# Performance work log

Hardware: AMD Instinct MI355X
Metric: run time of the kernel (lower is better)

Reference implementation:

```python
import jax, jax.numpy as jnp
import numpy as np

DIM = 256
HEADS = 8
DIM_HEAD = 64
INNER = HEADS * DIM_HEAD  # 512
SCALE = DIM_HEAD ** -0.5
EPS = 1e-5


def _layernorm(x, w, b):
    mu = jnp.mean(x, axis=-1, keepdims=True)
    var = jnp.var(x, axis=-1, keepdims=True)
    return (x - mu) * jax.lax.rsqrt(var + EPS) * w + b


def setup_inputs() -> dict:
    key = jax.random.key(0)
    ks = jax.random.split(key, 20)
    B, N, M, H, W = 8, 4096, 256, 64, 64
    s = 0.02
    inp = {
        "feat": jax.random.normal(ks[0], (B, N, DIM), jnp.float32),
        "center": jax.random.normal(ks[1], (B, M, DIM), jnp.float32),
        "pos": jax.random.normal(ks[2], (B, DIM, H, W), jnp.float32),
        "center_pos": jax.random.normal(ks[3], (B, M, DIM), jnp.float32),
        # projection weights stored [in, out] so y = x @ W
        "Wq": jax.random.normal(ks[4], (DIM, INNER), jnp.float32) * s,
        "Wk": jax.random.normal(ks[5], (DIM, INNER), jnp.float32) * s,
        "Wv1": jax.random.normal(ks[6], (DIM, INNER), jnp.float32) * s,
        "Wv2": jax.random.normal(ks[7], (DIM, INNER), jnp.float32) * s,
        "Wo1": jax.random.normal(ks[8], (INNER, DIM), jnp.float32) * s,
        "Wo2": jax.random.normal(ks[9], (INNER, DIM), jnp.float32) * s,
        "ln1_w": jnp.ones((DIM,), jnp.float32),
        "ln1_b": jnp.zeros((DIM,), jnp.float32),
        "ln2_w": jnp.ones((DIM,), jnp.float32),
        "ln2_b": jnp.zeros((DIM,), jnp.float32),
        "ffn1_W1": jax.random.normal(ks[10], (DIM, DIM), jnp.float32) * s,
        "ffn1_W2": jax.random.normal(ks[11], (DIM, DIM), jnp.float32) * s,
        "ffn1_b2": jnp.zeros((DIM,), jnp.float32),
        "ffn2_W1": jax.random.normal(ks[12], (DIM, DIM), jnp.float32) * s,
        "ffn2_W2": jax.random.normal(ks[13], (DIM, DIM), jnp.float32) * s,
        "ffn2_b2": jnp.zeros((DIM,), jnp.float32),
    }
    return inp


def reference(feat, center, pos, center_pos, Wq, Wk, Wv1, Wv2, Wo1, Wo2,
              ln1_w, ln1_b, ln2_w, ln2_b, ffn1_W1, ffn1_W2, ffn1_b2,
              ffn2_W1, ffn2_W2, ffn2_b2):
    B = feat.shape[0]
    # pos: [B, C, H, W] -> [B, N, C]
    pos_f = pos.reshape(B, DIM, -1).transpose(0, 2, 1)
    q = (feat + pos_f) @ Wq            # [B, N, INNER]
    k = (center + center_pos) @ Wk     # [B, M, INNER]
    v1 = feat @ Wv1                    # [B, N, INNER]
    v2 = center @ Wv2                  # [B, M, INNER]

    def split(x):  # [B, T, h*d] -> [B, h, T, d]
        return x.reshape(B, x.shape[1], HEADS, DIM_HEAD).transpose(0, 2, 1, 3)

    q, k, v1, v2 = split(q), split(k), split(v1), split(v2)
    attn = jnp.einsum("bhnd,bhmd->bhnm", q, k) * SCALE  # [B, h, N, M]
    attn1 = jax.nn.softmax(attn, axis=-2)  # over N (queries)
    attn2 = jax.nn.softmax(attn, axis=-1)  # over M (keys)
    out_feat = jnp.einsum("bhnm,bhmd->bhnd", attn2, v2)    # [B, h, N, d]
    out_center = jnp.einsum("bhnm,bhnd->bhmd", attn1, v1)  # [B, h, M, d]

    def merge(x):  # [B, h, T, d] -> [B, T, h*d]
        return x.transpose(0, 2, 1, 3).reshape(B, x.shape[2], INNER)

    out_feat = merge(out_feat) @ Wo1 + feat
    out_center = merge(out_center) @ Wo2 + center
    out_feat = _layernorm(out_feat, ln1_w, ln1_b)
    out_center = _layernorm(out_center, ln2_w, ln2_b)
    out_feat = jax.nn.relu(out_feat @ ffn1_W1) @ ffn1_W2 + ffn1_b2 + out_feat
    out_center = jax.nn.relu(out_center @ ffn2_W1) @ ffn2_W2 + ffn2_b2 + out_center
    return out_feat, out_center
```

## Files before the change

### kernel.cpp

```cpp
#include <hip/hip_runtime.h>

typedef __bf16 bf16;
typedef __bf16 bf16x4 __attribute__((ext_vector_type(4)));
typedef __bf16 bf16x8 __attribute__((ext_vector_type(8)));
typedef float f32x4 __attribute__((ext_vector_type(4)));

#define MFMA16(a, b, c) __builtin_amdgcn_mfma_f32_16x16x32_bf16(a, b, c, 0, 0, 0)

#define CEXP 0.18033688011112042f

struct WTArgs {
  const float* src[10];
  bf16* dst[10];
  int K[10];
  int N[10];
};

__global__ __launch_bounds__(256) void wtrans_kernel(WTArgs args) {
  const int z = blockIdx.z;
  const int K = args.K[z], N = args.N[z];
  const int k0 = blockIdx.x * 64, n0 = blockIdx.y * 64;
  if (k0 >= K || n0 >= N) return;
  __shared__ float t[64][65];
  const int tx = threadIdx.x & 63, ty = threadIdx.x >> 6;
  const float* __restrict__ src = args.src[z];
  bf16* __restrict__ dst = args.dst[z];
#pragma unroll
  for (int i = 0; i < 16; ++i)
    t[ty + i * 4][tx] = src[(size_t)(k0 + ty + i * 4) * N + n0 + tx];
  __syncthreads();
#pragma unroll
  for (int i = 0; i < 16; ++i)
    dst[(size_t)(n0 + ty + i * 4) * K + k0 + tx] = (bf16)t[tx][ty + i * 4];
}

__global__ __launch_bounds__(256) void prep_xq_kernel(
    const float* __restrict__ feat, const float* __restrict__ pos,
    bf16* __restrict__ xq) {
  const int n0 = blockIdx.x * 64;
  const int c0 = blockIdx.y * 64;
  const int b = blockIdx.z;
  __shared__ float t[64][65];
  const int tx = threadIdx.x & 63, ty = threadIdx.x >> 6;
#pragma unroll
  for (int i = 0; i < 16; ++i) {
    int c = ty + i * 4;
    t[c][tx] = pos[((size_t)b * 256 + c0 + c) * 4096 + n0 + tx];
  }
  __syncthreads();
#pragma unroll
  for (int i = 0; i < 16; ++i) {
    int n = ty + i * 4;
    size_t off = ((size_t)b * 4096 + n0 + n) * 256 + c0 + tx;
    xq[off] = (bf16)(feat[off] + t[tx][n]);
  }
}

__device__ inline void stage16(const bf16* g, bf16* l) {
  __builtin_amdgcn_global_load_lds(
      (const __attribute__((address_space(1))) void*)g,
      (__attribute__((address_space(3))) void*)l, 16, 0, 0);
}
__device__ inline void stage16(const float* g, bf16* l) {
  f32x4 u = *(const f32x4*)g;
  f32x4 v = *((const f32x4*)g + 1);
  bf16x8 o;
#pragma unroll
  for (int i = 0; i < 4; ++i) {
    o[i] = (bf16)u[i];
    o[4 + i] = (bf16)v[i];
  }
  *(bf16x8*)l = o;
}
__device__ inline void stage16(const float* g, const float* g2, bf16* l) {
  f32x4 u = *(const f32x4*)g + *(const f32x4*)g2;
  f32x4 v = *((const f32x4*)g + 1) + *((const f32x4*)g2 + 1);
  bf16x8 o;
#pragma unroll
  for (int i = 0; i < 4; ++i) {
    o[i] = (bf16)u[i];
    o[4 + i] = (bf16)v[i];
  }
  *(bf16x8*)l = o;
}

__device__ inline f32x4 rload(const float* p) { return *(const f32x4*)p; }
__device__ inline f32x4 rload(const bf16* p) {
  bf16x4 t = *(const bf16x4*)p;
  return (f32x4){(float)t[0], (float)t[1], (float)t[2], (float)t[3]};
}
__device__ inline void cstore(float* p, f32x4 v) { *(f32x4*)p = v; }
__device__ inline void cstore(bf16* p, f32x4 v) {
  bf16x4 o;
  o[0] = (bf16)v[0]; o[1] = (bf16)v[1]; o[2] = (bf16)v[2]; o[3] = (bf16)v[3];
  *(bf16x4*)p = o;
}

struct GArg {
  const void* A[2];
  const void* A2[2];
  const bf16* BT[2];
  void* C[2];
  const void* resid[2];
  const float* bias[2];
  int M[2];
};

template <int EPI, typename TO, typename TR, typename TA, bool FUSE2>
__global__ __launch_bounds__(256) void gemm_kernel(GArg g, int N, int K) {
  const int z = blockIdx.z;
  const int m0 = blockIdx.x * 128;
  if (m0 >= g.M[z]) return;
  const TA* A = (const TA*)g.A[z];
  const TA* A2 = (const TA*)g.A2[z];
  const bf16* BT = g.BT[z];
  TO* C = (TO*)g.C[z];
  const TR* resid = (const TR*)g.resid[z];
  const float* bias = g.bias[z];

  const int n0 = blockIdx.y * 128;
  const int tid = threadIdx.x;
  const int lane = tid & 63;
  const int w = tid >> 6;
  const int wr = (w >> 1) * 64, wc = (w & 1) * 64;
  const int l15 = lane & 15, quad = lane >> 4;

  __shared__ __align__(16) bf16 Al[128 * 32];
  __shared__ __align__(16) bf16 Bl[128 * 32];

  f32x4 acc[4][4];
#pragma unroll
  for (int i = 0; i < 4; ++i)
#pragma unroll
    for (int j = 0; j < 4; ++j) acc[i][j] = (f32x4){0.f, 0.f, 0.f, 0.f};

  const int sw = (((l15 >> 1) & 3) ^ quad) * 8;

  for (int k0 = 0; k0 < K; k0 += 32) {
#pragma unroll
    for (int c = 0; c < 2; ++c) {
      int idx = tid + c * 256;
      int row = idx >> 2;
      int gs = ((idx & 3) ^ ((row >> 1) & 3)) * 8;
      size_t aoff = (size_t)(m0 + row) * K + k0 + gs;
      if constexpr (FUSE2)
        stage16(A + aoff, A2 + aoff, Al + idx * 8);
      else
        stage16(A + aoff, Al + idx * 8);
      stage16(BT + (size_t)(n0 + row) * K + k0 + gs, Bl + idx * 8);
    }
    __syncthreads();
    bf16x8 fa[4], fb[4];
#pragma unroll
    for (int i = 0; i < 4; ++i) {
      fa[i] = *(const bf16x8*)(Al + (wr + i * 16 + l15) * 32 + sw);
      fb[i] = *(const bf16x8*)(Bl + (wc + i * 16 + l15) * 32 + sw);
    }
#pragma unroll
    for (int i = 0; i < 4; ++i)
#pragma unroll
      for (int j = 0; j < 4; ++j)
        acc[i][j] = MFMA16(fb[j], fa[i], acc[i][j]);
    __syncthreads();
  }

#pragma unroll
  for (int i = 0; i < 4; ++i) {
#pragma unroll
    for (int j = 0; j < 4; ++j) {
      int row = m0 + wr + i * 16 + l15;
      int col = n0 + wc + j * 16 + quad * 4;
      size_t off = (size_t)row * N + col;
      f32x4 v = acc[i][j];
      if constexpr (EPI == 1) {
#pragma unroll
        for (int e = 0; e < 4; ++e) v[e] = fmaxf(v[e], 0.f);
      }
      if constexpr (EPI == 2) v += rload(resid + off);
      if constexpr (EPI == 3)
        v += rload(resid + off) + *(const f32x4*)(bias + col);
      cstore(C + off, v);
    }
  }
}

__global__ __launch_bounds__(256, 1) void attf_kernel(
    const bf16* q, const bf16* __restrict__ kk, const bf16* __restrict__ v1,
    const bf16* __restrict__ v2, bf16* af, float* __restrict__ acc_p,
    float* __restrict__ colsum_p) {
  const int nb = blockIdx.x;
  const int h = blockIdx.y;
  const int b = blockIdx.z;
  const int tid = threadIdx.x;
  const int lane = tid & 63;
  const int w = tid >> 6;
  const int l15 = lane & 15, quad = lane >> 4;

  __shared__ __align__(16) bf16 klds[256 * 72];
  __shared__ __align__(16) bf16 v2T[64 * 264];
  __shared__ __align__(16) bf16 v1T[2][64 * 72];
  __shared__ __align__(16) bf16 PT[256 * 72];
  __shared__ __align__(16) bf16 Pl[4][16 * 264];

#pragma unroll
  for (int c = 0; c < 8; ++c) {
    int idx = tid + c * 256;
    int m = idx >> 3;
    int dc = (idx & 7) * 8;
    *(bf16x8*)(klds + m * 72 + dc) =
        *(const bf16x8*)(kk + ((size_t)(b * 256 + m)) * 512 + h * 64 + dc);
  }
#pragma unroll
  for (int c = 0; c < 8; ++c) {
    int idx = tid + c * 256;
    int m = idx >> 3;
    int dc = (idx & 7) * 8;
    bf16x8 t =
        *(const bf16x8*)(v2 + ((size_t)(b * 256 + m)) * 512 + h * 64 + dc);
#pragma unroll
    for (int j = 0; j < 8; ++j) v2T[(dc + j) * 264 + m] = t[j];
  }
  {
    const int nl = tid >> 3;
    const int dc = (tid & 7) * 8;
    const bf16* v1b =
        v1 + ((size_t)(b * 4096 + nb * 1024)) * 512 + h * 64 + dc;
    bf16x8 t0 = *(const bf16x8*)(v1b + (size_t)nl * 512);
    bf16x8 t1 = *(const bf16x8*)(v1b + (size_t)(nl + 32) * 512);
#pragma unroll
    for (int j = 0; j < 8; ++j) {
      v1T[0][(dc + j) * 72 + nl] = t0[j];
      v1T[0][(dc + j) * 72 + nl + 32] = t1[j];
    }
  }
  bf16x8 qa0, qa1;
  {
    int nrow = b * 4096 + nb * 1024 + w * 16 + l15;
    const bf16* qp = q + (size_t)nrow * 512 + h * 64 + quad * 8;
    qa0 = *(const bf16x8*)(qp);
    qa1 = *(const bf16x8*)(qp + 32);
  }

  f32x4 oc2[16];
#pragma unroll
  for (int i = 0; i < 16; ++i) oc2[i] = (f32x4){0.f, 0.f, 0.f, 0.f};
  float cs[16];
#pragma unroll
  for (int i = 0; i < 16; ++i) cs[i] = 0.f;

  __syncthreads();

#pragma unroll 2
  for (int ch = 0; ch < 16; ++ch) {
    bf16x8 v1a, v1b;
    const int nl = tid >> 3;
    const int dc = (tid & 7) * 8;
    if (ch < 15) {
      const bf16* v1p =
          v1 + ((size_t)(b * 4096 + nb * 1024 + (ch + 1) * 64)) * 512 +
          h * 64 + dc;
      v1a = *(const bf16x8*)(v1p + (size_t)nl * 512);
      v1b = *(const bf16x8*)(v1p + (size_t)(nl + 32) * 512);
    }

    float rs[4] = {0.f, 0.f, 0.f, 0.f};
#pragma unroll
    for (int mt = 0; mt < 16; ++mt) {
      const bf16* kp = klds + (mt * 16 + l15) * 72 + quad * 8;
      bf16x8 b0 = *(const bf16x8*)(kp);
      bf16x8 b1 = *(const bf16x8*)(kp + 32);
      f32x4 s = (f32x4){0.f, 0.f, 0.f, 0.f};
      s = MFMA16(qa0, b0, s);
      s = MFMA16(qa1, b1, s);
      float e0 = exp2f(s[0] * CEXP);
      float e1 = exp2f(s[1] * CEXP);
      float e2 = exp2f(s[2] * CEXP);
      float e3 = exp2f(s[3] * CEXP);
      rs[0] += e0; rs[1] += e1; rs[2] += e2; rs[3] += e3;
      cs[mt] += e0 + e1 + e2 + e3;
      Pl[w][(quad * 4 + 0) * 264 + mt * 16 + l15] = (bf16)e0;
      Pl[w][(quad * 4 + 1) * 264 + mt * 16 + l15] = (bf16)e1;
      Pl[w][(quad * 4 + 2) * 264 + mt * 16 + l15] = (bf16)e2;
      Pl[w][(quad * 4 + 3) * 264 + mt * 16 + l15] = (bf16)e3;
      bf16x4 ev;
      ev[0] = (bf16)e0; ev[1] = (bf16)e1; ev[2] = (bf16)e2; ev[3] = (bf16)e3;
      *(bf16x4*)(PT + (mt * 16 + l15) * 72 + w * 16 + quad * 4) = ev;
    }
    if (ch < 15) {
      bf16* dst = v1T[(ch + 1) & 1];
#pragma unroll
      for (int j = 0; j < 8; ++j) {
        dst[(dc + j) * 72 + nl] = v1a[j];
        dst[(dc + j) * 72 + nl + 32] = v1b[j];
      }
    }
    __syncthreads();

    bf16x8 qn0 = qa0, qn1 = qa1;
    if (ch < 15) {
      int nrow = b * 4096 + nb * 1024 + (ch + 1) * 64 + w * 16 + l15;
      const bf16* qp = q + (size_t)nrow * 512 + h * 64 + quad * 8;
      qn0 = *(const bf16x8*)(qp);
      qn1 = *(const bf16x8*)(qp + 32);
    }

    f32x4 o1[4];
#pragma unroll
    for (int i = 0; i < 4; ++i) o1[i] = (f32x4){0.f, 0.f, 0.f, 0.f};
#pragma unroll
    for (int ks = 0; ks < 8; ++ks) {
      bf16x8 pa = *(const bf16x8*)(Pl[w] + l15 * 264 + ks * 32 + quad * 8);
#pragma unroll
      for (int dt = 0; dt < 4; ++dt) {
        bf16x8 vb = *(const bf16x8*)(v2T + (dt * 16 + l15) * 264 + ks * 32 +
                                     quad * 8);
        o1[dt] = MFMA16(vb, pa, o1[dt]);
      }
    }
#pragma unroll
    for (int r = 0; r < 4; ++r) {
      float v = rs[r];
      v += __shfl_xor(v, 1, 64);
      v += __shfl_xor(v, 2, 64);
      v += __shfl_xor(v, 4, 64);
      v += __shfl_xor(v, 8, 64);
      rs[r] = v;
    }
    {
      int srcq = (l15 >> 2) << 4;
      float s0 = __shfl(rs[0], srcq, 64);
      float s1 = __shfl(rs[1], srcq, 64);
      float s2 = __shfl(rs[2], srcq, 64);
      float s3 = __shfl(rs[3], srcq, 64);
      float a01 = (l15 & 1) ? s1 : s0;
      float a23 = (l15 & 1) ? s3 : s2;
      float inv = 1.f / ((l15 & 2) ? a23 : a01);
      int n = nb * 1024 + ch * 64 + w * 16 + l15;
      bf16* ap = af + ((size_t)(b * 4096 + n)) * 512 + h * 64 + quad * 4;
#pragma unroll
      for (int dt = 0; dt < 4; ++dt) {
        bf16x4 ov;
        ov[0] = (bf16)(o1[dt][0] * inv);
        ov[1] = (bf16)(o1[dt][1] * inv);
        ov[2] = (bf16)(o1[dt][2] * inv);
        ov[3] = (bf16)(o1[dt][3] * inv);
        *(bf16x4*)(ap + dt * 16) = ov;
      }
    }

    const bf16* vc = v1T[ch & 1];
#pragma unroll
    for (int ks = 0; ks < 2; ++ks) {
      bf16x8 vbv[4];
#pragma unroll
      for (int dt = 0; dt < 4; ++dt)
        vbv[dt] = *(const bf16x8*)(vc + (dt * 16 + l15) * 72 + ks * 32 +
                                   quad * 8);
#pragma unroll
      for (int mq = 0; mq < 4; ++mq) {
        bf16x8 pa2 = *(const bf16x8*)(PT + (mq * 64 + w * 16 + l15) * 72 +
                                      ks * 32 + quad * 8);
#pragma unroll
        for (int dt = 0; dt < 4; ++dt)
          oc2[mq * 4 + dt] = MFMA16(vbv[dt], pa2, oc2[mq * 4 + dt]);
      }
    }
    __syncthreads();
    qa0 = qn0;
    qa1 = qn1;
  }

  float* cw = (float*)klds;
#pragma unroll
  for (int t = 0; t < 16; ++t) {
    float v = cs[t];
    v += __shfl_xor(v, 16, 64);
    v += __shfl_xor(v, 32, 64);
    if (quad == 0) cw[w * 256 + t * 16 + l15] = v;
  }
  __syncthreads();
  {
    int m = tid;
    float s = cw[m] + cw[256 + m] + cw[512 + m] + cw[768 + m];
    colsum_p[((size_t)(nb * 64 + b * 8 + h)) * 256 + m] = s;
  }
  float* base = acc_p + ((size_t)(nb * 64 + b * 8 + h)) * 256 * 64;
#pragma unroll
  for (int mq = 0; mq < 4; ++mq) {
    int m = mq * 64 + w * 16 + l15;
#pragma unroll
    for (int dt = 0; dt < 4; ++dt)
      *(f32x4*)(base + m * 64 + dt * 16 + quad * 4) = oc2[mq * 4 + dt];
  }
}

__global__ __launch_bounds__(256) void acm_kernel(
    const float* __restrict__ acc_p, const float* __restrict__ colsum_p,
    bf16* __restrict__ acm) {
  int idx = blockIdx.x * 256 + threadIdx.x;
  int d = idx & 63;
  int h = (idx >> 6) & 7;
  int m = (idx >> 9) & 255;
  int b = idx >> 17;
  float cv = 0.f, v = 0.f;
#pragma unroll
  for (int p = 0; p < 4; ++p) {
    cv += colsum_p[((size_t)(p * 64 + b * 8 + h)) * 256 + m];
    v += acc_p[(((size_t)(p * 64 + b * 8 + h)) * 256 + m) * 64 + d];
  }
  acm[idx] = (bf16)(v / cv);
}

__global__ __launch_bounds__(256) void ln_kernel(
    const bf16* __restrict__ x0, const bf16* __restrict__ x1,
    const float* __restrict__ w0, const float* __restrict__ b0,
    const float* __restrict__ w1, const float* __restrict__ b1,
    bf16* __restrict__ y0, bf16* __restrict__ y1, int rows0, int rows1) {
  int wave = threadIdx.x >> 6;
  int lane = threadIdx.x & 63;
  int row = blockIdx.x * 4 + wave;
  const bf16* x;
  const float *wv, *bv;
  bf16* y;
  if (row < rows0) {
    x = x0; wv = w0; bv = b0; y = y0;
  } else {
    row -= rows0;
    if (row >= rows1) return;
    x = x1; wv = w1; bv = b1; y = y1;
  }
  const bf16* xr = x + (size_t)row * 256;
  bf16x4 v = *(const bf16x4*)(xr + lane * 4);
  float f0 = v[0], f1 = v[1], f2 = v[2], f3 = v[3];
  float s = f0 + f1 + f2 + f3;
  float ss = f0 * f0 + f1 * f1 + f2 * f2 + f3 * f3;
#pragma unroll
  for (int m = 1; m < 64; m <<= 1) {
    s += __shfl_xor(s, m, 64);
    ss += __shfl_xor(ss, m, 64);
  }
  float mean = s * (1.f / 256.f);
  float var = ss * (1.f / 256.f) - mean * mean;
  float rstd = rsqrtf(var + 1e-5f);
  f32x4 wq = *(const f32x4*)(wv + lane * 4);
  f32x4 bq = *(const f32x4*)(bv + lane * 4);
  bf16x4 o;
  o[0] = (bf16)((f0 - mean) * rstd * wq[0] + bq[0]);
  o[1] = (bf16)((f1 - mean) * rstd * wq[1] + bq[1]);
  o[2] = (bf16)((f2 - mean) * rstd * wq[2] + bq[2]);
  o[3] = (bf16)((f3 - mean) * rstd * wq[3] + bq[3]);
  *(bf16x4*)(y + (size_t)row * 256 + lane * 4) = o;
}

extern "C" void kernel_launch(void* const* d_in, const int* in_sizes, int n_in,
                              void* d_out, int out_size, void* d_ws,
                              size_t ws_size, hipStream_t stream) {
  const float* feat = (const float*)d_in[0];
  const float* center = (const float*)d_in[1];
  const float* pos = (const float*)d_in[2];
  const float* cpos = (const float*)d_in[3];
  const float* Wq = (const float*)d_in[4];
  const float* Wk = (const float*)d_in[5];
  const float* Wv1 = (const float*)d_in[6];
  const float* Wv2 = (const float*)d_in[7];
  const float* Wo1 = (const float*)d_in[8];
  const float* Wo2 = (const float*)d_in[9];
  const float* ln1w = (const float*)d_in[10];
  const float* ln1b = (const float*)d_in[11];
  const float* ln2w = (const float*)d_in[12];
  const float* ln2b = (const float*)d_in[13];
  const float* f1W1 = (const float*)d_in[14];
  const float* f1W2 = (const float*)d_in[15];
  const float* f1b2 = (const float*)d_in[16];
  const float* f2W1 = (const float*)d_in[17];
  const float* f2W2 = (const float*)d_in[18];
  const float* f2b2 = (const float*)d_in[19];

  char* ws = (char*)d_ws;
  const size_t MB = 1024 * 1024;
  bf16* q_ = (bf16*)(ws + 0);
  bf16* af_ = q_;
  bf16* v1_ = (bf16*)(ws + 32 * MB);
  bf16* xq_ = (bf16*)(ws + 64 * MB);
  float* accp_ = (float*)(ws + 64 * MB);
  bf16* rf_ = xq_;
  bf16* k_ = (bf16*)(ws + 80 * MB);
  bf16* rc_ = (bf16*)(ws + 82 * MB);
  bf16* v2_ = (bf16*)(ws + 83 * MB);
  bf16* acm_ = v2_;
  float* colsum_ = (float*)(ws + 89 * MB);
  bf16* wt_ = (bf16*)(ws + 89 * MB + 262144);
  bf16* yf_ = q_;
  bf16* tf_ = (bf16*)(ws + 16 * MB);
  bf16* yc_ = (bf16*)(ws + 92 * MB);
  bf16* tc_ = (bf16*)(ws + 93 * MB);

  bf16* WqT = wt_;
  bf16* WkT = WqT + 131072;
  bf16* Wv1T = WkT + 131072;
  bf16* Wv2T = Wv1T + 131072;
  bf16* Wo1T = Wv2T + 131072;
  bf16* Wo2T = Wo1T + 131072;
  bf16* f1W1T = Wo2T + 131072;
  bf16* f1W2T = f1W1T + 65536;
  bf16* f2W1T = f1W2T + 65536;
  bf16* f2W2T = f2W1T + 65536;

  float* out_feat = (float*)d_out;
  float* out_center = out_feat + (size_t)8 * 4096 * 256;

  WTArgs wa;
  const float* srcs[10] = {Wq, Wk, Wv1, Wv2, Wo1, Wo2, f1W1, f1W2, f2W1, f2W2};
  bf16* dsts[10] = {WqT, WkT, Wv1T, Wv2T, Wo1T, Wo2T, f1W1T, f1W2T, f2W1T, f2W2T};
  int Ks[10] = {256, 256, 256, 256, 512, 512, 256, 256, 256, 256};
  int Ns[10] = {512, 512, 512, 512, 256, 256, 256, 256, 256, 256};
  for (int i = 0; i < 10; ++i) {
    wa.src[i] = srcs[i];
    wa.dst[i] = dsts[i];
    wa.K[i] = Ks[i];
    wa.N[i] = Ns[i];
  }

  wtrans_kernel<<<dim3(8, 8, 10), 256, 0, stream>>>(wa);
  prep_xq_kernel<<<dim3(64, 4, 8), 256, 0, stream>>>(feat, pos, xq_);

  {
    GArg a{};
    a.A[0] = xq_; a.BT[0] = WqT; a.C[0] = q_; a.M[0] = 32768;
    gemm_kernel<0, bf16, bf16, bf16, false>
        <<<dim3(256, 4, 1), 256, 0, stream>>>(a, 512, 256);
  }
  {
    GArg a{};
    a.A[0] = center; a.A2[0] = cpos; a.BT[0] = WkT; a.C[0] = k_;
    a.M[0] = 2048;
    gemm_kernel<0, bf16, bf16, float, true>
        <<<dim3(16, 4, 1), 256, 0, stream>>>(a, 512, 256);
  }
  {
    GArg a{};
    a.A[0] = feat; a.A[1] = center;
    a.BT[0] = Wv1T; a.BT[1] = Wv2T;
    a.C[0] = v1_; a.C[1] = v2_;
    a.M[0] = 32768; a.M[1] = 2048;
    gemm_kernel<0, bf16, bf16, float, false>
        <<<dim3(256, 4, 2), 256, 0, stream>>>(a, 512, 256);
  }

  attf_kernel<<<dim3(4, 8, 8), 256, 0, stream>>>(q_, k_, v1_, v2_, af_, accp_,
                                                 colsum_);
  acm_kernel<<<dim3(4096), 256, 0, stream>>>(accp_, colsum_, acm_);

  {
    GArg a{};
    a.A[0] = af_; a.A[1] = acm_;
    a.BT[0] = Wo1T; a.BT[1] = Wo2T;
    a.C[0] = rf_; a.C[1] = rc_;
    a.resid[0] = feat; a.resid[1] = center;
    a.M[0] = 32768; a.M[1] = 2048;
    gemm_kernel<2, bf16, float, bf16, false>
        <<<dim3(256, 2, 2), 256, 0, stream>>>(a, 256, 512);
  }
  ln_kernel<<<dim3(8704), 256, 0, stream>>>(rf_, rc_, ln1w, ln1b, ln2w, ln2b,
                                            yf_, yc_, 32768, 2048);
  {
    GArg a{};
    a.A[0] = yf_; a.A[1] = yc_;
    a.BT[0] = f1W1T; a.BT[1] = f2W1T;
    a.C[0] = tf_; a.C[1] = tc_;
    a.M[0] = 32768; a.M[1] = 2048;
    gemm_kernel<1, bf16, bf16, bf16, false>
        <<<dim3(256, 2, 2), 256, 0, stream>>>(a, 256, 256);
  }
  {
    GArg a{};
    a.A[0] = tf_; a.A[1] = tc_;
    a.BT[0] = f1W2T; a.BT[1] = f2W2T;
    a.C[0] = out_feat; a.C[1] = out_center;
    a.resid[0] = yf_; a.resid[1] = yc_;
    a.bias[0] = f1b2; a.bias[1] = f2b2;
    a.M[0] = 32768; a.M[1] = 2048;
    gemm_kernel<3, float, bf16, bf16, false>
        <<<dim3(256, 2, 2), 256, 0, stream>>>(a, 256, 256);
  }
}
```

Before: 379.6 us.

## Double-buffer GEMM LDS tiles and keep attention probabilities in registers

The GEMM kernel now double-buffers its A/B LDS tiles, so each k-step needs one barrier instead of two and the next tile's loads can overlap the MFMAs. In the attention kernel the S MFMA operands are swapped so each lane holds the probabilities it needs for the P·V2 product in registers. v2T is stored with a permuted column order to match, and the Pl shared buffer and the cross-lane row-sum shuffles are removed. Column sums are now computed by an MFMA against a ones vector instead of per-lane accumulation plus an LDS reduction, at the cost of extra MFMAs and higher register pressure.

```diff
diff --git a/kernel.cpp b/kernel.cpp
--- a/kernel.cpp
+++ b/kernel.cpp
@@ -125,8 +125,8 @@
   const int wr = (w >> 1) * 64, wc = (w & 1) * 64;
   const int l15 = lane & 15, quad = lane >> 4;
 
-  __shared__ __align__(16) bf16 Al[128 * 32];
-  __shared__ __align__(16) bf16 Bl[128 * 32];
+  __shared__ __align__(16) bf16 Al[2][128 * 32];
+  __shared__ __align__(16) bf16 Bl[2][128 * 32];
 
   f32x4 acc[4][4];
 #pragma unroll
@@ -136,7 +136,7 @@
 
   const int sw = (((l15 >> 1) & 3) ^ quad) * 8;
 
-  for (int k0 = 0; k0 < K; k0 += 32) {
+  auto stage = [&](int buf, int k0) {
 #pragma unroll
     for (int c = 0; c < 2; ++c) {
       int idx = tid + c * 256;
@@ -144,24 +144,31 @@
       int gs = ((idx & 3) ^ ((row >> 1) & 3)) * 8;
       size_t aoff = (size_t)(m0 + row) * K + k0 + gs;
       if constexpr (FUSE2)
-        stage16(A + aoff, A2 + aoff, Al + idx * 8);
+        stage16(A + aoff, A2 + aoff, Al[buf] + idx * 8);
       else
-        stage16(A + aoff, Al + idx * 8);
-      stage16(BT + (size_t)(n0 + row) * K + k0 + gs, Bl + idx * 8);
-    }
+        stage16(A + aoff, Al[buf] + idx * 8);
+      stage16(BT + (size_t)(n0 + row) * K + k0 + gs, Bl[buf] + idx * 8);
+    }
+  };
+
+  stage(0, 0);
+  int cur = 0;
+  const int nt = K >> 5;
+  for (int t = 0; t < nt; ++t) {
     __syncthreads();
+    if (t + 1 < nt) stage(cur ^ 1, (t + 1) * 32);
     bf16x8 fa[4], fb[4];
 #pragma unroll
     for (int i = 0; i < 4; ++i) {
-      fa[i] = *(const bf16x8*)(Al + (wr + i * 16 + l15) * 32 + sw);
-      fb[i] = *(const bf16x8*)(Bl + (wc + i * 16 + l15) * 32 + sw);
+      fa[i] = *(const bf16x8*)(Al[cur] + (wr + i * 16 + l15) * 32 + sw);
+      fb[i] = *(const bf16x8*)(Bl[cur] + (wc + i * 16 + l15) * 32 + sw);
     }
 #pragma unroll
     for (int i = 0; i < 4; ++i)
 #pragma unroll
       for (int j = 0; j < 4; ++j)
         acc[i][j] = MFMA16(fb[j], fa[i], acc[i][j]);
-    __syncthreads();
+    cur ^= 1;
   }
 
 #pragma unroll
@@ -200,7 +207,6 @@
   __shared__ __align__(16) bf16 v2T[64 * 264];
   __shared__ __align__(16) bf16 v1T[2][64 * 72];
   __shared__ __align__(16) bf16 PT[256 * 72];
-  __shared__ __align__(16) bf16 Pl[4][16 * 264];
 
 #pragma unroll
   for (int c = 0; c < 8; ++c) {
@@ -217,8 +223,10 @@
     int dc = (idx & 7) * 8;
     bf16x8 t =
         *(const bf16x8*)(v2 + ((size_t)(b * 256 + m)) * 512 + h * 64 + dc);
-#pragma unroll
-    for (int j = 0; j < 8; ++j) v2T[(dc + j) * 264 + m] = t[j];
+    int p = (m & ~31) |
+            (((((m >> 2) & 3) << 3) + (m & 3)) + (((m >> 4) & 1) << 2));
+#pragma unroll
+    for (int j = 0; j < 8; ++j) v2T[(dc + j) * 264 + p] = t[j];
   }
   {
     const int nl = tid >> 3;
@@ -244,13 +252,15 @@
   f32x4 oc2[16];
 #pragma unroll
   for (int i = 0; i < 16; ++i) oc2[i] = (f32x4){0.f, 0.f, 0.f, 0.f};
-  float cs[16];
-#pragma unroll
-  for (int i = 0; i < 16; ++i) cs[i] = 0.f;
+  f32x4 csa[4];
+#pragma unroll
+  for (int i = 0; i < 4; ++i) csa[i] = (f32x4){0.f, 0.f, 0.f, 0.f};
+  bf16x8 ones8;
+#pragma unroll
+  for (int j = 0; j < 8; ++j) ones8[j] = (bf16)1.0f;
 
   __syncthreads();
 
-#pragma unroll 2
   for (int ch = 0; ch < 16; ++ch) {
     bf16x8 v1a, v1b;
     const int nl = tid >> 3;
@@ -263,45 +273,31 @@
       v1b = *(const bf16x8*)(v1p + (size_t)(nl + 32) * 512);
     }
 
-    float rs[4] = {0.f, 0.f, 0.f, 0.f};
+    bf16x8 pa[8];
+    float rs = 0.f;
 #pragma unroll
     for (int mt = 0; mt < 16; ++mt) {
       const bf16* kp = klds + (mt * 16 + l15) * 72 + quad * 8;
-      bf16x8 b0 = *(const bf16x8*)(kp);
-      bf16x8 b1 = *(const bf16x8*)(kp + 32);
+      bf16x8 ka0 = *(const bf16x8*)(kp);
+      bf16x8 ka1 = *(const bf16x8*)(kp + 32);
       f32x4 s = (f32x4){0.f, 0.f, 0.f, 0.f};
-      s = MFMA16(qa0, b0, s);
-      s = MFMA16(qa1, b1, s);
+      s = MFMA16(ka0, qa0, s);
+      s = MFMA16(ka1, qa1, s);
       float e0 = exp2f(s[0] * CEXP);
       float e1 = exp2f(s[1] * CEXP);
       float e2 = exp2f(s[2] * CEXP);
       float e3 = exp2f(s[3] * CEXP);
-      rs[0] += e0; rs[1] += e1; rs[2] += e2; rs[3] += e3;
-      cs[mt] += e0 + e1 + e2 + e3;
-      Pl[w][(quad * 4 + 0) * 264 + mt * 16 + l15] = (bf16)e0;
-      Pl[w][(quad * 4 + 1) * 264 + mt * 16 + l15] = (bf16)e1;
-      Pl[w][(quad * 4 + 2) * 264 + mt * 16 + l15] = (bf16)e2;
-      Pl[w][(quad * 4 + 3) * 264 + mt * 16 + l15] = (bf16)e3;
-      bf16x4 ev;
-      ev[0] = (bf16)e0; ev[1] = (bf16)e1; ev[2] = (bf16)e2; ev[3] = (bf16)e3;
-      *(bf16x4*)(PT + (mt * 16 + l15) * 72 + w * 16 + quad * 4) = ev;
-    }
-    if (ch < 15) {
-      bf16* dst = v1T[(ch + 1) & 1];
-#pragma unroll
-      for (int j = 0; j < 8; ++j) {
-        dst[(dc + j) * 72 + nl] = v1a[j];
-        dst[(dc + j) * 72 + nl + 32] = v1b[j];
-      }
-    }
-    __syncthreads();
-
-    bf16x8 qn0 = qa0, qn1 = qa1;
-    if (ch < 15) {
-      int nrow = b * 4096 + nb * 1024 + (ch + 1) * 64 + w * 16 + l15;
-      const bf16* qp = q + (size_t)nrow * 512 + h * 64 + quad * 8;
-      qn0 = *(const bf16x8*)(qp);
-      qn1 = *(const bf16x8*)(qp + 32);
+      rs += (e0 + e1) + (e2 + e3);
+      bf16 b0 = (bf16)e0, b1 = (bf16)e1, b2 = (bf16)e2, b3 = (bf16)e3;
+      int mrow = mt * 16 + quad * 4;
+      PT[(mrow + 0) * 72 + w * 16 + l15] = b0;
+      PT[(mrow + 1) * 72 + w * 16 + l15] = b1;
+      PT[(mrow + 2) * 72 + w * 16 + l15] = b2;
+      PT[(mrow + 3) * 72 + w * 16 + l15] = b3;
+      pa[mt >> 1][(mt & 1) * 4 + 0] = b0;
+      pa[mt >> 1][(mt & 1) * 4 + 1] = b1;
+      pa[mt >> 1][(mt & 1) * 4 + 2] = b2;
+      pa[mt >> 1][(mt & 1) * 4 + 3] = b3;
     }
 
     f32x4 o1[4];
@@ -309,32 +305,17 @@
     for (int i = 0; i < 4; ++i) o1[i] = (f32x4){0.f, 0.f, 0.f, 0.f};
 #pragma unroll
     for (int ks = 0; ks < 8; ++ks) {
-      bf16x8 pa = *(const bf16x8*)(Pl[w] + l15 * 264 + ks * 32 + quad * 8);
 #pragma unroll
       for (int dt = 0; dt < 4; ++dt) {
         bf16x8 vb = *(const bf16x8*)(v2T + (dt * 16 + l15) * 264 + ks * 32 +
                                      quad * 8);
-        o1[dt] = MFMA16(vb, pa, o1[dt]);
+        o1[dt] = MFMA16(vb, pa[ks], o1[dt]);
       }
     }
-#pragma unroll
-    for (int r = 0; r < 4; ++r) {
-      float v = rs[r];
-      v += __shfl_xor(v, 1, 64);
-      v += __shfl_xor(v, 2, 64);
-      v += __shfl_xor(v, 4, 64);
-      v += __shfl_xor(v, 8, 64);
-      rs[r] = v;
-    }
     {
-      int srcq = (l15 >> 2) << 4;
-      float s0 = __shfl(rs[0], srcq, 64);
-      float s1 = __shfl(rs[1], srcq, 64);
-      float s2 = __shfl(rs[2], srcq, 64);
-      float s3 = __shfl(rs[3], srcq, 64);
-      float a01 = (l15 & 1) ? s1 : s0;
-      float a23 = (l15 & 1) ? s3 : s2;
-      float inv = 1.f / ((l15 & 2) ? a23 : a01);
+      float rsf = rs + __shfl_xor(rs, 16, 64);
+      rsf += __shfl_xor(rsf, 32, 64);
+      float inv = 1.f / rsf;
       int n = nb * 1024 + ch * 64 + w * 16 + l15;
       bf16* ap = af + ((size_t)(b * 4096 + n)) * 512 + h * 64 + quad * 4;
 #pragma unroll
@@ -348,6 +329,24 @@
       }
     }
 
+    if (ch < 15) {
+      bf16* dst = v1T[(ch + 1) & 1];
+#pragma unroll
+      for (int j = 0; j < 8; ++j) {
+        dst[(dc + j) * 72 + nl] = v1a[j];
+        dst[(dc + j) * 72 + nl + 32] = v1b[j];
+      }
+    }
+    __syncthreads();
+
+    bf16x8 qn0 = qa0, qn1 = qa1;
+    if (ch < 15) {
+      int nrow = b * 4096 + nb * 1024 + (ch + 1) * 64 + w * 16 + l15;
+      const bf16* qp = q + (size_t)nrow * 512 + h * 64 + quad * 8;
+      qn0 = *(const bf16x8*)(qp);
+      qn1 = *(const bf16x8*)(qp + 32);
+    }
+
     const bf16* vc = v1T[ch & 1];
 #pragma unroll
     for (int ks = 0; ks < 2; ++ks) {
@@ -363,6 +362,7 @@
 #pragma unroll
         for (int dt = 0; dt < 4; ++dt)
           oc2[mq * 4 + dt] = MFMA16(vbv[dt], pa2, oc2[mq * 4 + dt]);
+        csa[mq] = MFMA16(pa2, ones8, csa[mq]);
       }
     }
     __syncthreads();
@@ -370,21 +370,15 @@
     qa1 = qn1;
   }
 
-  float* cw = (float*)klds;
-#pragma unroll
-  for (int t = 0; t < 16; ++t) {
-    float v = cs[t];
-    v += __shfl_xor(v, 16, 64);
-    v += __shfl_xor(v, 32, 64);
-    if (quad == 0) cw[w * 256 + t * 16 + l15] = v;
-  }
-  __syncthreads();
-  {
-    int m = tid;
-    float s = cw[m] + cw[256 + m] + cw[512 + m] + cw[768 + m];
-    colsum_p[((size_t)(nb * 64 + b * 8 + h)) * 256 + m] = s;
-  }
-  float* base = acc_p + ((size_t)(nb * 64 + b * 8 + h)) * 256 * 64;
+  const size_t slab = (size_t)(nb * 64 + b * 8 + h);
+  if (l15 == 0) {
+#pragma unroll
+    for (int mq = 0; mq < 4; ++mq)
+#pragma unroll
+      for (int r = 0; r < 4; ++r)
+        colsum_p[slab * 256 + mq * 64 + w * 16 + quad * 4 + r] = csa[mq][r];
+  }
+  float* base = acc_p + slab * (256 * 64);
 #pragma unroll
   for (int mq = 0; mq < 4; ++mq) {
     int m = mq * 64 + w * 16 + l15;
```

New measurement: 359.2 us. 5.4% less time.
